# Kernel tuning notes

Hardware: AMD Instinct MI355X
Metric: run time of the kernel (lower is better)

## Reference

```python
import jax, jax.numpy as jnp
import numpy as np

B, C, H, W = 4, 4, 1080, 1920


def setup_inputs() -> dict:
    key = jax.random.key(0)
    k1, k2 = jax.random.split(key)
    frame = jax.random.normal(k1, (B, C, H, W), dtype=jnp.float32)
    flow = jax.random.normal(k2, (B, 2, H, W), dtype=jnp.float32)
    return {"frame": frame, "flow": flow}


def _bilinear_warp(frame, flow):
    # TF-addons style dense_image_warp: sample frame at (y - flow_y, x - flow_x),
    # query points clamped to the image rectangle, bilinear interpolation.
    b, c, h, w = frame.shape
    gy = jnp.arange(h, dtype=flow.dtype)
    gx = jnp.arange(w, dtype=flow.dtype)
    qy = jnp.clip(gy[None, :, None] - flow[:, 0], 0.0, h - 1)  # [B,H,W]
    qx = jnp.clip(gx[None, None, :] - flow[:, 1], 0.0, w - 1)  # [B,H,W]
    y0f = jnp.floor(qy)
    x0f = jnp.floor(qx)
    wy = (qy - y0f)[:, None]  # [B,1,H,W]
    wx = (qx - x0f)[:, None]
    y0 = y0f.astype(jnp.int32)
    x0 = x0f.astype(jnp.int32)
    y1 = jnp.minimum(y0 + 1, h - 1)
    x1 = jnp.minimum(x0 + 1, w - 1)
    ff = frame.reshape(b, c, h * w)

    def gather(y, x):
        idx = (y * w + x).reshape(b, 1, h * w)
        return jnp.take_along_axis(ff, idx, axis=2).reshape(b, c, h, w)

    top = gather(y0, x0) * (1.0 - wx) + gather(y0, x1) * wx
    bot = gather(y1, x0) * (1.0 - wx) + gather(y1, x1) * wx
    return top * (1.0 - wy) + bot * wy


def reference(frame, flow):
    return _bilinear_warp(frame, flow)
```

## Files before the change

kernel.cpp:

```cpp
#include <hip/hip_runtime.h>


#define BB 4
#define CC 4
#define HH 1080
#define WW 1920
#define HW (HH * WW)
#define NPX (BB * HH * WW)
#define NBLK (NPX / 256)
#define WS_BYTES ((size_t)NPX * CC * 2)

typedef _Float16 h4 __attribute__((ext_vector_type(4), aligned(8)));
typedef _Float16 h8 __attribute__((ext_vector_type(8), aligned(8)));

__global__ __launch_bounds__(256) void nhwc_fp16_prepass(
    const float* __restrict__ frame,
    _Float16* __restrict__ ws)
{
    const int n   = blockIdx.x;
    const int blk = (n & 7) * (NBLK >> 3) + (n >> 3);
    const int p   = blk * 256 + threadIdx.x;
    const int x = p % WW;
    const int t = p / WW;
    const int y = t % HH;
    const int b = t / HH;

    const size_t off = (size_t)(b * CC) * HW + (size_t)y * WW + x;
    h4 o;
    o[0] = (_Float16)frame[off];
    o[1] = (_Float16)frame[off + (size_t)HW];
    o[2] = (_Float16)frame[off + (size_t)(2 * HW)];
    o[3] = (_Float16)frame[off + (size_t)(3 * HW)];
    *reinterpret_cast<h4*>(ws + (size_t)p * 4) = o;
}

__global__ __launch_bounds__(256) void dense_warp_gather(
    const _Float16* __restrict__ ws,
    const float* __restrict__ flow,
    float* __restrict__ out)
{
    const int n   = blockIdx.x;
    const int blk = (n & 7) * (NBLK >> 3) + (n >> 3);
    const int p   = blk * 256 + threadIdx.x;
    const int x = p % WW;
    const int t = p / WW;
    const int y = t % HH;
    const int b = t / HH;

    const size_t rowoff = (size_t)y * WW + x;
    const float fy = flow[(size_t)(b * 2 + 0) * HW + rowoff];
    const float fx = flow[(size_t)(b * 2 + 1) * HW + rowoff];

    const float qy  = fminf(fmaxf((float)y - fy, 0.0f), (float)(HH - 1));
    const float qx  = fminf(fmaxf((float)x - fx, 0.0f), (float)(WW - 1));
    const float y0f = floorf(qy);
    const float x0f = floorf(qx);
    const float wy  = qy - y0f;
    float       wx  = qx - x0f;
    const int y0 = (int)y0f;
    const int x0 = (int)x0f;
    const int y1 = min(y0 + 1, HH - 1);

    const bool edge = (x0 > WW - 2);
    const int  xb   = edge ? (WW - 2) : x0;
    if (edge) wx = 1.0f;

    const h8 tp = *reinterpret_cast<const h8*>(
        ws + ((size_t)(b * HH + y0) * WW + xb) * 4);
    const h8 bt = *reinterpret_cast<const h8*>(
        ws + ((size_t)(b * HH + y1) * WW + xb) * 4);

    const float omwx = 1.0f - wx;
    const float omwy = 1.0f - wy;

#pragma unroll
    for (int c = 0; c < CC; ++c) {
        const float tl = (float)tp[c];
        const float tr = (float)tp[c + 4];
        const float bl = (float)bt[c];
        const float br = (float)bt[c + 4];
        const float top = tl * omwx + tr * wx;
        const float bot = bl * omwx + br * wx;
        const float v   = top * omwy + bot * wy;
        __builtin_nontemporal_store(v, out + (size_t)(b * CC + c) * HW + rowoff);
    }
}

typedef float f32x2 __attribute__((ext_vector_type(2), aligned(4)));

__global__ __launch_bounds__(256) void dense_warp_fallback(
    const float* __restrict__ frame,
    const float* __restrict__ flow,
    float* __restrict__ out)
{
    const int n   = blockIdx.x;
    const int blk = (n & 7) * (NBLK >> 3) + (n >> 3);
    const int p   = blk * 256 + threadIdx.x;
    const int x = p % WW;
    const int t = p / WW;
    const int y = t % HH;
    const int b = t / HH;

    const size_t rowoff = (size_t)y * WW + x;
    const float fy = flow[(size_t)(b * 2 + 0) * HW + rowoff];
    const float fx = flow[(size_t)(b * 2 + 1) * HW + rowoff];

    const float qy  = fminf(fmaxf((float)y - fy, 0.0f), (float)(HH - 1));
    const float qx  = fminf(fmaxf((float)x - fx, 0.0f), (float)(WW - 1));
    const float y0f = floorf(qy);
    const float x0f = floorf(qx);
    const float wy  = qy - y0f;
    float       wx  = qx - x0f;
    const int y0 = (int)y0f;
    const int x0 = (int)x0f;
    const int y1 = min(y0 + 1, HH - 1);
    const bool edge = (x0 > WW - 2);
    const int  xb   = edge ? (WW - 2) : x0;
    if (edge) wx = 1.0f;

    const int i0 = y0 * WW + xb;
    const int i1 = y1 * WW + xb;
    const float omwx = 1.0f - wx;
    const float omwy = 1.0f - wy;

#pragma unroll
    for (int c = 0; c < CC; ++c) {
        const float* fp = frame + (size_t)(b * CC + c) * HW;
        const f32x2 t2 = *reinterpret_cast<const f32x2*>(fp + i0);
        const f32x2 b2 = *reinterpret_cast<const f32x2*>(fp + i1);
        const float top = t2.x * omwx + t2.y * wx;
        const float bot = b2.x * omwx + b2.y * wx;
        const float v   = top * omwy + bot * wy;
        __builtin_nontemporal_store(v, out + (size_t)(b * CC + c) * HW + rowoff);
    }
}

extern "C" void kernel_launch(void* const* d_in, const int* in_sizes, int n_in,
                              void* d_out, int out_size, void* d_ws, size_t ws_size,
                              hipStream_t stream)
{
    const float* frame = (const float*)d_in[0];
    const float* flow  = (const float*)d_in[1];
    float* out = (float*)d_out;

    if (ws_size >= WS_BYTES && d_ws != nullptr) {
        _Float16* ws = (_Float16*)d_ws;
        nhwc_fp16_prepass<<<NBLK, 256, 0, stream>>>(frame, ws);
        dense_warp_gather<<<NBLK, 256, 0, stream>>>(ws, flow, out);
    } else {
        dense_warp_fallback<<<NBLK, 256, 0, stream>>>(frame, flow, out);
    }
}
```

Before: 69.91 us.

## Tile gather kernel into 128x12 blocks and vectorize prepass to two pixels

The gather kernel now assigns each block a 128-wide by 12-row tile, with each thread looping over six rows. The aim is to improve 2D locality of the gathered fp16 NHWC workspace in cache and to amortize index math. The prepass now converts two pixels per thread using float2 loads and 16-byte stores, halving its grid. The trade-offs are fewer blocks in flight for the gather and more serialized work per thread.

Result: no change. 71.23 us (+1.9%).

```diff
diff --git a/kernel.cpp b/kernel.cpp
--- a/kernel.cpp
+++ b/kernel.cpp
@@ -7,31 +7,40 @@
 #define WW 1920
 #define HW (HH * WW)
 #define NPX (BB * HH * WW)
-#define NBLK (NPX / 256)
 #define WS_BYTES ((size_t)NPX * CC * 2)
 
-typedef _Float16 h4 __attribute__((ext_vector_type(4), aligned(8)));
+#define TW 128
+#define TH 12
+#define TILES_X (WW / TW)
+#define TILES_Y (HH / TH)
+#define NBLK_G (BB * TILES_Y * TILES_X)
+
+#define NBLK_P (NPX / 2 / 256)
+
 typedef _Float16 h8 __attribute__((ext_vector_type(8), aligned(8)));
+typedef float f32x2 __attribute__((ext_vector_type(2), aligned(4)));
 
 __global__ __launch_bounds__(256) void nhwc_fp16_prepass(
     const float* __restrict__ frame,
     _Float16* __restrict__ ws)
 {
     const int n   = blockIdx.x;
-    const int blk = (n & 7) * (NBLK >> 3) + (n >> 3);
-    const int p   = blk * 256 + threadIdx.x;
+    const int blk = (n & 7) * (NBLK_P >> 3) + (n >> 3);
+    const int p   = (blk * 256 + threadIdx.x) * 2;
     const int x = p % WW;
     const int t = p / WW;
     const int y = t % HH;
     const int b = t / HH;
 
     const size_t off = (size_t)(b * CC) * HW + (size_t)y * WW + x;
-    h4 o;
-    o[0] = (_Float16)frame[off];
-    o[1] = (_Float16)frame[off + (size_t)HW];
-    o[2] = (_Float16)frame[off + (size_t)(2 * HW)];
-    o[3] = (_Float16)frame[off + (size_t)(3 * HW)];
-    *reinterpret_cast<h4*>(ws + (size_t)p * 4) = o;
+    h8 o;
+#pragma unroll
+    for (int c = 0; c < CC; ++c) {
+        const f32x2 v = *reinterpret_cast<const f32x2*>(frame + off + (size_t)c * HW);
+        o[c]     = (_Float16)v.x;
+        o[c + 4] = (_Float16)v.y;
+    }
+    *reinterpret_cast<h8*>(ws + (size_t)p * 4) = o;
 }
 
 __global__ __launch_bounds__(256) void dense_warp_gather(
@@ -40,53 +49,65 @@
     float* __restrict__ out)
 {
     const int n   = blockIdx.x;
-    const int blk = (n & 7) * (NBLK >> 3) + (n >> 3);
-    const int p   = blk * 256 + threadIdx.x;
-    const int x = p % WW;
-    const int t = p / WW;
-    const int y = t % HH;
-    const int b = t / HH;
+    const int blk = (n & 7) * (NBLK_G >> 3) + (n >> 3);
 
-    const size_t rowoff = (size_t)y * WW + x;
-    const float fy = flow[(size_t)(b * 2 + 0) * HW + rowoff];
-    const float fx = flow[(size_t)(b * 2 + 1) * HW + rowoff];
+    const int txi = blk % TILES_X;
+    const int t2  = blk / TILES_X;
+    const int tyi = t2 % TILES_Y;
+    const int b   = t2 / TILES_Y;
 
-    const float qy  = fminf(fmaxf((float)y - fy, 0.0f), (float)(HH - 1));
-    const float qx  = fminf(fmaxf((float)x - fx, 0.0f), (float)(WW - 1));
-    const float y0f = floorf(qy);
-    const float x0f = floorf(qx);
-    const float wy  = qy - y0f;
-    float       wx  = qx - x0f;
-    const int y0 = (int)y0f;
-    const int x0 = (int)x0f;
-    const int y1 = min(y0 + 1, HH - 1);
+    const int x     = txi * TW + (threadIdx.x & (TW - 1));
+    const int rg    = threadIdx.x >> 7;
+    const int ybase = tyi * TH + rg * (TH / 2);
 
-    const bool edge = (x0 > WW - 2);
-    const int  xb   = edge ? (WW - 2) : x0;
-    if (edge) wx = 1.0f;
-
-    const h8 tp = *reinterpret_cast<const h8*>(
-        ws + ((size_t)(b * HH + y0) * WW + xb) * 4);
-    const h8 bt = *reinterpret_cast<const h8*>(
-        ws + ((size_t)(b * HH + y1) * WW + xb) * 4);
-
-    const float omwx = 1.0f - wx;
-    const float omwy = 1.0f - wy;
+    const float* __restrict__ flowy = flow + (size_t)(b * 2) * HW;
+    const float* __restrict__ flowx = flowy + HW;
+    const _Float16* __restrict__ wsb = ws + (size_t)b * HW * 4;
+    float* __restrict__ outb = out + (size_t)(b * CC) * HW;
 
 #pragma unroll
-    for (int c = 0; c < CC; ++c) {
-        const float tl = (float)tp[c];
-        const float tr = (float)tp[c + 4];
-        const float bl = (float)bt[c];
-        const float br = (float)bt[c + 4];
-        const float top = tl * omwx + tr * wx;
-        const float bot = bl * omwx + br * wx;
-        const float v   = top * omwy + bot * wy;
-        __builtin_nontemporal_store(v, out + (size_t)(b * CC + c) * HW + rowoff);
+    for (int r = 0; r < TH / 2; ++r) {
+        const int y = ybase + r;
+        const size_t rowoff = (size_t)y * WW + x;
+
+        const float fy = flowy[rowoff];
+        const float fx = flowx[rowoff];
+
+        const float qy  = fminf(fmaxf((float)y - fy, 0.0f), (float)(HH - 1));
+        const float qx  = fminf(fmaxf((float)x - fx, 0.0f), (float)(WW - 1));
+        const float y0f = floorf(qy);
+        const float x0f = floorf(qx);
+        const float wy  = qy - y0f;
+        float       wx  = qx - x0f;
+        const int y0 = (int)y0f;
+        const int x0 = (int)x0f;
+        const int y1 = min(y0 + 1, HH - 1);
+
+        const bool edge = (x0 > WW - 2);
+        const int  xb   = edge ? (WW - 2) : x0;
+        if (edge) wx = 1.0f;
+
+        const h8 tp = *reinterpret_cast<const h8*>(wsb + ((size_t)y0 * WW + xb) * 4);
+        const h8 bt = *reinterpret_cast<const h8*>(wsb + ((size_t)y1 * WW + xb) * 4);
+
+        const float omwx = 1.0f - wx;
+        const float omwy = 1.0f - wy;
+
+#pragma unroll
+        for (int c = 0; c < CC; ++c) {
+            const float tl = (float)tp[c];
+            const float tr = (float)tp[c + 4];
+            const float bl = (float)bt[c];
+            const float br = (float)bt[c + 4];
+            const float top = tl * omwx + tr * wx;
+            const float bot = bl * omwx + br * wx;
+            const float v   = top * omwy + bot * wy;
+            __builtin_nontemporal_store(v, outb + (size_t)c * HW + rowoff);
+        }
     }
 }
 
-typedef float f32x2 __attribute__((ext_vector_type(2), aligned(4)));
+#define NBLK_F (NPX / 256)
 
 __global__ __launch_bounds__(256) void dense_warp_fallback(
     const float* __restrict__ frame,
@@ -94,7 +115,7 @@
     float* __restrict__ out)
 {
     const int n   = blockIdx.x;
-    const int blk = (n & 7) * (NBLK >> 3) + (n >> 3);
+    const int blk = (n & 7) * (NBLK_F >> 3) + (n >> 3);
     const int p   = blk * 256 + threadIdx.x;
     const int x = p % WW;
     const int t = p / WW;
@@ -145,9 +166,9 @@
 
     if (ws_size >= WS_BYTES && d_ws != nullptr) {
         _Float16* ws = (_Float16*)d_ws;
-        nhwc_fp16_prepass<<<NBLK, 256, 0, stream>>>(frame, ws);
-        dense_warp_gather<<<NBLK, 256, 0, stream>>>(ws, flow, out);
+        nhwc_fp16_prepass<<<NBLK_P, 256, 0, stream>>>(frame, ws);
+        dense_warp_gather<<<NBLK_G, 256, 0, stream>>>(ws, flow, out);
     } else {
-        dense_warp_fallback<<<NBLK, 256, 0, stream>>>(frame, flow, out);
+        dense_warp_fallback<<<NBLK_F, 256, 0, stream>>>(frame, flow, out);
     }
 }
```
